# Optimization experiments

Hardware: AMD Instinct MI355X
Metric: run time of the kernel (lower is better)

Reference implementation:

```python
import jax, jax.numpy as jnp
import numpy as np

T = 16384
J = 21
IN = 3 * J + 278  # 341
H = 512
WIDTH = 64


def _gru_cell(x, h, w_ih, w_hh, b_ih, b_n):
    # equinox GRUCell math: igates = W_ih x + b; hgates = W_hh h
    ig = w_ih @ x + b_ih            # [3H]
    hg = w_hh @ h                   # [3H]
    ir, iz, inn = jnp.split(ig, 3)
    hr, hz, hn = jnp.split(hg, 3)
    r = jax.nn.sigmoid(ir + hr)
    z = jax.nn.sigmoid(iz + hz)
    n = jnp.tanh(inn + r * (hn + b_n))
    return n + z * (h - n)


def setup_inputs() -> dict:
    key = jax.random.key(0)
    ks = jax.random.split(key, 32)
    s = 0.02
    inp = {
        'dh_joint_pos_tj': jax.random.normal(ks[0], (T, J), jnp.float32),
        'dh_joint_vel_tj': jax.random.normal(ks[1], (T, J), jnp.float32),
        'com_inertia_tn': jax.random.normal(ks[2], (T, 160), jnp.float32),
        'com_vel_tn': jax.random.normal(ks[3], (T, 96), jnp.float32),
        'imu_acc_t3': jax.random.normal(ks[4], (T, 3), jnp.float32),
        'imu_gyro_t3': jax.random.normal(ks[5], (T, 3), jnp.float32),
        'act_frc_obs_tn': jax.random.normal(ks[6], (T, J), jnp.float32),
        'base_pos_t3': jax.random.normal(ks[7], (T, 3), jnp.float32),
        'base_quat_t4': jax.random.normal(ks[8], (T, 4), jnp.float32),
        'lin_vel_obs_t3': jax.random.normal(ks[9], (T, 3), jnp.float32),
        'ang_vel_obs_t3': jax.random.normal(ks[10], (T, 3), jnp.float32),
        'lin_vel_cmd_t2': jax.random.normal(ks[11], (T, 2), jnp.float32),
        'ang_vel_cmd_t1': jax.random.normal(ks[12], (T, 1), jnp.float32),
        'hidden_states_dn': jnp.zeros((2, H), jnp.float32),
        # GRU layer 0 (input IN -> H)
        'w_ih0': jax.random.normal(ks[13], (3 * H, IN), jnp.float32) * s,
        'w_hh0': jax.random.normal(ks[14], (3 * H, H), jnp.float32) * s,
        'b_ih0': jax.random.normal(ks[15], (3 * H,), jnp.float32) * s,
        'b_n0': jax.random.normal(ks[16], (H,), jnp.float32) * s,
        # GRU layer 1 (H -> H)
        'w_ih1': jax.random.normal(ks[17], (3 * H, H), jnp.float32) * s,
        'w_hh1': jax.random.normal(ks[18], (3 * H, H), jnp.float32) * s,
        'b_ih1': jax.random.normal(ks[19], (3 * H,), jnp.float32) * s,
        'b_n1': jax.random.normal(ks[20], (H,), jnp.float32) * s,
        # projector MLP: H -> 64 -> 64 -> 1, relu hidden activations
        'mw0': jax.random.normal(ks[21], (WIDTH, H), jnp.float32) * s,
        'mb0': jnp.zeros((WIDTH,), jnp.float32),
        'mw1': jax.random.normal(ks[22], (WIDTH, WIDTH), jnp.float32) * s,
        'mb1': jnp.zeros((WIDTH,), jnp.float32),
        'mw2': jax.random.normal(ks[23], (1, WIDTH), jnp.float32) * s,
        'mb2': jnp.zeros((1,), jnp.float32),
    }
    return inp


def reference(dh_joint_pos_tj, dh_joint_vel_tj, com_inertia_tn, com_vel_tn,
              imu_acc_t3, imu_gyro_t3, act_frc_obs_tn, base_pos_t3,
              base_quat_t4, lin_vel_obs_t3, ang_vel_obs_t3, lin_vel_cmd_t2,
              ang_vel_cmd_t1, hidden_states_dn,
              w_ih0, w_hh0, b_ih0, b_n0, w_ih1, w_hh1, b_ih1, b_n1,
              mw0, mb0, mw1, mb1, mw2, mb2):
    obs_tn = jnp.concatenate([
        dh_joint_pos_tj, dh_joint_vel_tj, com_inertia_tn, com_vel_tn,
        imu_acc_t3, imu_gyro_t3, act_frc_obs_tn, base_pos_t3, base_quat_t4,
        lin_vel_obs_t3, ang_vel_obs_t3, lin_vel_cmd_t2, ang_vel_cmd_t1,
    ], axis=-1)  # [T, 341]

    def scan_fn(carry, xt):
        h0 = _gru_cell(xt, carry[0], w_ih0, w_hh0, b_ih0, b_n0)
        h1 = _gru_cell(h0, carry[1], w_ih1, w_hh1, b_ih1, b_n1)
        v = jax.nn.relu(mw0 @ h1 + mb0)
        v = jax.nn.relu(mw1 @ v + mb1)
        yt = mw2 @ v + mb2  # [1]
        return jnp.stack([h0, h1], axis=0), yt

    new_hidden, out_tn = jax.lax.scan(scan_fn, hidden_states_dn, obs_tn)
    return out_tn, new_hidden
```

## Files before the change

kernel.cpp:

```cpp
#include <hip/hip_runtime.h>
#include <math.h>


#define T_STEPS 16384
#define IN_DIM 341
#define HID 512
#define G3 1536
#define TTILE 16
#define R0 16
#define R0M (R0-1)
#define R1 16
#define R1M (R1-1)

typedef unsigned int v4u __attribute__((ext_vector_type(4)));

__device__ __forceinline__ float dot4(float4 a, float4 b) {
  return fmaf(a.x, b.x, fmaf(a.y, b.y, fmaf(a.z, b.z, a.w * b.w)));
}
__device__ __forceinline__ float fast_sigmoid(float x) {
  return __builtin_amdgcn_rcpf(1.0f + __expf(-x));
}
__device__ __forceinline__ float fast_tanh(float x) {
  return fmaf(-2.0f, __builtin_amdgcn_rcpf(1.0f + __expf(2.0f * x)), 1.0f);
}
__device__ __forceinline__ void st_rlx64(unsigned long long* p, unsigned long long v) {
  __hip_atomic_store(p, v, __ATOMIC_RELAXED, __HIP_MEMORY_SCOPE_AGENT);
}
__device__ __forceinline__ unsigned long long pack_tv(unsigned tag, float v) {
  return ((unsigned long long)tag << 32) | (unsigned long long)__float_as_uint(v);
}
__device__ __forceinline__ void pin4(float4& v) {
  asm volatile("" : "+v"(v.x), "+v"(v.y), "+v"(v.z), "+v"(v.w));
}
__device__ __forceinline__ v4u ld16(const unsigned long long* p) {
  v4u r;
  asm volatile("global_load_dwordx4 %0, %1, off sc0 sc1\n\ts_waitcnt vmcnt(0)"
               : "=v"(r) : "v"(p) : "memory");
  return r;
}
__device__ __forceinline__ void ld16x2(const unsigned long long* p0,
                                       const unsigned long long* p1,
                                       v4u& a, v4u& b) {
  asm volatile("global_load_dwordx4 %0, %2, off sc0 sc1\n\t"
               "global_load_dwordx4 %1, %3, off sc0 sc1\n\t"
               "s_waitcnt vmcnt(0)"
               : "=v"(a), "=v"(b) : "v"(p0), "v"(p1) : "memory");
}

__global__ __launch_bounds__(384) void concat_kernel(
    const float* __restrict__ p0, const float* __restrict__ p1,
    const float* __restrict__ p2, const float* __restrict__ p3,
    const float* __restrict__ p4, const float* __restrict__ p5,
    const float* __restrict__ p6, const float* __restrict__ p7,
    const float* __restrict__ p8, const float* __restrict__ p9,
    const float* __restrict__ p10, const float* __restrict__ p11,
    const float* __restrict__ p12, float* __restrict__ obs) {
  int t = blockIdx.x;
  int k = threadIdx.x;
  if (k >= IN_DIM) return;
  float v;
  if (k < 21)       v = p0[t*21 + k];
  else if (k < 42)  v = p1[t*21 + (k-21)];
  else if (k < 202) v = p2[t*160 + (k-42)];
  else if (k < 298) v = p3[t*96 + (k-202)];
  else if (k < 301) v = p4[t*3 + (k-298)];
  else if (k < 304) v = p5[t*3 + (k-301)];
  else if (k < 325) v = p6[t*21 + (k-304)];
  else if (k < 328) v = p7[t*3 + (k-325)];
  else if (k < 332) v = p8[t*4 + (k-328)];
  else if (k < 335) v = p9[t*3 + (k-332)];
  else if (k < 338) v = p10[t*3 + (k-335)];
  else if (k < 340) v = p11[t*2 + (k-338)];
  else              v = p12[t];
  obs[(size_t)t*IN_DIM + k] = v;
}

__global__ __launch_bounds__(256) void transpose_kernel(const float* __restrict__ w,
                                                        float* __restrict__ wT) {
  __shared__ float tile[32][33];
  int tx = threadIdx.x;
  int ty = threadIdx.y;
  int k = blockIdx.x*32 + tx;
#pragma unroll
  for (int jj = 0; jj < 4; jj++) {
    int r = blockIdx.y*32 + ty*4 + jj;
    tile[ty*4+jj][tx] = (k < IN_DIM) ? w[(size_t)r*IN_DIM + k] : 0.f;
  }
  __syncthreads();
#pragma unroll
  for (int jj = 0; jj < 4; jj++) {
    int kk = blockIdx.x*32 + ty*4 + jj;
    if (kk < IN_DIM) wT[(size_t)kk*G3 + blockIdx.y*32 + tx] = tile[tx][ty*4+jj];
  }
}

__global__ __launch_bounds__(256) void ig0_kernel(const float* __restrict__ wT,
                                                  const float* __restrict__ obs,
                                                  const float* __restrict__ b_ih0,
                                                  float* __restrict__ ig0) {
  int o = blockIdx.x*256 + threadIdx.x;
  int t0 = blockIdx.y * TTILE;
  float acc[TTILE];
  float b = b_ih0[o];
#pragma unroll
  for (int tt = 0; tt < TTILE; tt++) acc[tt] = b;
  for (int k = 0; k < IN_DIM; k++) {
    float wv = wT[(size_t)k*G3 + o];
#pragma unroll
    for (int tt = 0; tt < TTILE; tt++)
      acc[tt] = fmaf(obs[(size_t)(t0+tt)*IN_DIM + k], wv, acc[tt]);
  }
#pragma unroll
  for (int tt = 0; tt < TTILE; tt++)
    ig0[(size_t)(t0+tt)*G3 + o] = acc[tt];
}

__global__ __launch_bounds__(512) void init_kernel(const float* __restrict__ hid,
                                                   unsigned long long* ring0,
                                                   unsigned long long* ring1) {
  int e = threadIdx.x;
  st_rlx64(&ring0[e], pack_tv(0u, hid[e]));
  st_rlx64(&ring1[e], pack_tv(0u, hid[HID + e]));
}

__global__ __launch_bounds__(384)
__attribute__((amdgpu_waves_per_eu(1, 2)))
void seq_kernel(
    const float* __restrict__ ig0, const float* __restrict__ w_hh0,
    const float* __restrict__ b_n0, const float* __restrict__ w_ih1,
    const float* __restrict__ w_hh1, const float* __restrict__ b_ih1,
    const float* __restrict__ b_n1,
    unsigned long long* ring0, unsigned long long* ring1,
    float* __restrict__ h1a, float* __restrict__ d_out) {
  __shared__ float hbuf0[2][HID];
  __shared__ float hbuf1[2][HID];
  __shared__ float igbuf[2][24];
  __shared__ float vpad[24576];
  const int tid = threadIdx.x;
  const int wg = blockIdx.x;
  if (d_out == nullptr) {
    vpad[tid] = (float)tid;
    __syncthreads();
    h1a[tid] = vpad[383 - tid];
  }

  const bool roleA = (tid < 128);
  const int u = tid - 128;
  const int g = roleA ? (tid >> 4) : (u >> 5);
  const int jj = roleA ? (tid & 15) : (u & 15);
  const int half = roleA ? 0 : ((u >> 4) & 1);
  const int j32 = roleA ? 0 : (u & 31);
  const int eg = wg*8 + g;
  const bool leadA = roleA && (jj == 0);
  const bool leadB = (!roleA) && (j32 == 0);

  const float* wsrc = roleA ? w_hh0 : (half ? w_hh1 : w_ih1);
  float4 W[24];
#pragma unroll
  for (int gate = 0; gate < 3; gate++) {
    const float4* row = (const float4*)(wsrc + (size_t)(gate*HID + eg)*HID);
#pragma unroll
    for (int i = 0; i < 8; i++) {
      W[gate*8+i] = row[jj + 16*i];
      pin4(W[gate*8+i]);
    }
  }
  float cr=0.f, cz=0.f, cn=0.f, bnl;
  if (roleA) {
    bnl = b_n0[eg];
  } else {
    cr = b_ih1[eg]; cz = b_ih1[512+eg]; cn = b_ih1[1024+eg]; bnl = b_n1[eg];
  }

  const int iggate = tid >> 3, ige = tid & 7;
  if (tid < 24) igbuf[0][tid] = ig0[(size_t)iggate*HID + wg*8 + ige];

  for (int k = 0; k <= T_STEPS; k++) {
    const int p = k & 1;
    float igpre = 0.f;
    if (tid < 24) {
      int kk = (k+1 < T_STEPS) ? (k+1) : (T_STEPS-1);
      igpre = ig0[(size_t)kk*G3 + (size_t)iggate*HID + wg*8 + ige];
    }
    const unsigned wk0 = (unsigned)k, wk1 = (unsigned)(k-1);
    if (k == 0) {
      if (tid < 256) {
        const unsigned long long* pa = ring0 + 2*tid;
        v4u a = ld16(pa);
        while (a.y != wk0 || a.w != wk0) { __builtin_amdgcn_s_sleep(1); a = ld16(pa); }
        ((float2*)hbuf0[p])[tid] =
            make_float2(__uint_as_float(a.x), __uint_as_float(a.z));
      }
    } else {
      const unsigned long long* pa = ring0 + (size_t)(k & R0M)*HID + 2*tid;
      const unsigned long long* pb = ring1 + (size_t)((k-1) & R1M)*HID + 2*(tid-128);
      if (tid < 128) {
        v4u a = ld16(pa);
        while (a.y != wk0 || a.w != wk0) { __builtin_amdgcn_s_sleep(1); a = ld16(pa); }
        ((float2*)hbuf0[p])[tid] =
            make_float2(__uint_as_float(a.x), __uint_as_float(a.z));
      } else if (tid < 256) {
        v4u a, b;
        ld16x2(pa, pb, a, b);
        while (a.y != wk0 || a.w != wk0) { __builtin_amdgcn_s_sleep(1); a = ld16(pa); }
        while (b.y != wk1 || b.w != wk1) { __builtin_amdgcn_s_sleep(1); b = ld16(pb); }
        ((float2*)hbuf0[p])[tid] =
            make_float2(__uint_as_float(a.x), __uint_as_float(a.z));
        ((float2*)hbuf1[p])[tid-128] =
            make_float2(__uint_as_float(b.x), __uint_as_float(b.z));
      } else {
        v4u b = ld16(pb);
        while (b.y != wk1 || b.w != wk1) { __builtin_amdgcn_s_sleep(1); b = ld16(pb); }
        ((float2*)hbuf1[p])[tid-128] =
            make_float2(__uint_as_float(b.x), __uint_as_float(b.z));
      }
    }
    __syncthreads();
    const bool act = roleA ? (k < T_STEPS) : (k >= 1);
    if (act) {
      const float4* hp = (roleA || half == 0) ? (const float4*)hbuf0[p]
                                              : (const float4*)hbuf1[p];
      float pr=0.f, pz=0.f, pn=0.f;
#pragma unroll
      for (int i = 0; i < 8; i++) {
        float4 hv = hp[jj + 16*i];
        pr += dot4(W[i],hv); pz += dot4(W[8+i],hv); pn += dot4(W[16+i],hv);
      }
#pragma unroll
      for (int s = 1; s < 16; s <<= 1) {
        pr += __shfl_xor(pr, s, 16);
        pz += __shfl_xor(pz, s, 16);
        pn += __shfl_xor(pn, s, 16);
      }
      if (roleA) {
        if (leadA) {
          float r = fast_sigmoid(igbuf[p][g] + pr);
          float z = fast_sigmoid(igbuf[p][8+g] + pz);
          float n = fast_tanh(igbuf[p][16+g] + r*(pn + bnl));
          float hnew = n + z*(hbuf0[p][eg] - n);
          st_rlx64(&ring0[(size_t)((k+1) & R0M)*HID + eg],
                   pack_tv((unsigned)(k+1), hnew));
          if (k == T_STEPS-1) d_out[T_STEPS + eg] = hnew;
        }
      } else {
        float qr = __shfl(pr, 16, 32);
        float qz = __shfl(pz, 16, 32);
        float qn = __shfl(pn, 16, 32);
        if (leadB) {
          float r = fast_sigmoid(pr + cr + qr);
          float z = fast_sigmoid(pz + cz + qz);
          float n = fast_tanh(pn + cn + r*(qn + bnl));
          float hnew = n + z*(hbuf1[p][eg] - n);
          st_rlx64(&ring1[(size_t)(k & R1M)*HID + eg],
                   pack_tv((unsigned)k, hnew));
          h1a[(size_t)(k-1)*HID + eg] = hnew;
          if (k == T_STEPS) d_out[T_STEPS + HID + eg] = hnew;
        }
      }
    }
    if (tid < 24) igbuf[p ^ 1][tid] = igpre;
  }
}

__global__ __launch_bounds__(64) void mlp_kernel(
    const float* __restrict__ h1_all, const float* __restrict__ mw0,
    const float* __restrict__ mb0, const float* __restrict__ mw1,
    const float* __restrict__ mb1, const float* __restrict__ mw2,
    const float* __restrict__ mb2, float* __restrict__ out) {
  const int l = threadIdx.x;
  const int t0 = blockIdx.x * 8;
  __shared__ float v0s[8][64];
  float acc[8];
#pragma unroll
  for (int tt = 0; tt < 8; tt++) acc[tt] = mb0[l];
  const float4* w = (const float4*)(mw0 + (size_t)l*512);
#pragma unroll 4
  for (int i = 0; i < 128; i++) {
    float4 a = w[i];
#pragma unroll
    for (int tt = 0; tt < 8; tt++) {
      float4 b = ((const float4*)(h1_all + (size_t)(t0+tt)*512))[i];
      acc[tt] = fmaf(a.x,b.x, fmaf(a.y,b.y, fmaf(a.z,b.z, fmaf(a.w,b.w, acc[tt]))));
    }
  }
#pragma unroll
  for (int tt = 0; tt < 8; tt++) v0s[tt][l] = fmaxf(acc[tt], 0.f);
  __syncthreads();
  float acc1[8];
#pragma unroll
  for (int tt = 0; tt < 8; tt++) acc1[tt] = mb1[l];
  const float* w1 = mw1 + (size_t)l*64;
  for (int jj = 0; jj < 64; jj++) {
    float wv = w1[jj];
#pragma unroll
    for (int tt = 0; tt < 8; tt++) acc1[tt] = fmaf(wv, v0s[tt][jj], acc1[tt]);
  }
  float w2 = mw2[l];
  float bb = mb2[0];
#pragma unroll
  for (int tt = 0; tt < 8; tt++) {
    float y = w2 * fmaxf(acc1[tt], 0.f);
#pragma unroll
    for (int s = 32; s > 0; s >>= 1) y += __shfl_down(y, s, 64);
    if (l == 0) out[t0+tt] = y + bb;
  }
}

extern "C" void kernel_launch(void* const* d_in, const int* in_sizes, int n_in,
                              void* d_out, int out_size, void* d_ws, size_t ws_size,
                              hipStream_t stream) {
  const float* p0  = (const float*)d_in[0];
  const float* p1  = (const float*)d_in[1];
  const float* p2  = (const float*)d_in[2];
  const float* p3  = (const float*)d_in[3];
  const float* p4  = (const float*)d_in[4];
  const float* p5  = (const float*)d_in[5];
  const float* p6  = (const float*)d_in[6];
  const float* p7  = (const float*)d_in[7];
  const float* p8  = (const float*)d_in[8];
  const float* p9  = (const float*)d_in[9];
  const float* p10 = (const float*)d_in[10];
  const float* p11 = (const float*)d_in[11];
  const float* p12 = (const float*)d_in[12];
  const float* hid   = (const float*)d_in[13];
  const float* w_ih0 = (const float*)d_in[14];
  const float* w_hh0 = (const float*)d_in[15];
  const float* b_ih0 = (const float*)d_in[16];
  const float* b_n0  = (const float*)d_in[17];
  const float* w_ih1 = (const float*)d_in[18];
  const float* w_hh1 = (const float*)d_in[19];
  const float* b_ih1 = (const float*)d_in[20];
  const float* b_n1  = (const float*)d_in[21];
  const float* mw0 = (const float*)d_in[22];
  const float* mb0 = (const float*)d_in[23];
  const float* mw1 = (const float*)d_in[24];
  const float* mb1 = (const float*)d_in[25];
  const float* mw2 = (const float*)d_in[26];
  const float* mb2 = (const float*)d_in[27];
  float* out = (float*)d_out;

  char* base = (char*)d_ws;
  const size_t IG0_B = (size_t)T_STEPS*G3*4;
  const size_t R0_B  = (size_t)R0*HID*8;
  const size_t R1_B  = (size_t)R1*HID*8;
  const size_t H1A_B = (size_t)T_STEPS*HID*4;
  float* ig0 = (float*)base;
  unsigned long long* ring0 = (unsigned long long*)(base + IG0_B);
  unsigned long long* ring1 = (unsigned long long*)(base + IG0_B + R0_B);
  float* h1a = (float*)(base + IG0_B + R0_B + R1_B);
  float* obs = h1a;
  float* wT  = (float*)((char*)h1a + (size_t)T_STEPS*IN_DIM*4);
  if (ws_size < IG0_B + R0_B + R1_B + H1A_B) return;

  concat_kernel<<<T_STEPS, 384, 0, stream>>>(p0,p1,p2,p3,p4,p5,p6,p7,p8,p9,p10,p11,p12, obs);
  transpose_kernel<<<dim3(11,48), dim3(32,8), 0, stream>>>(w_ih0, wT);
  ig0_kernel<<<dim3(6, T_STEPS/TTILE), 256, 0, stream>>>(wT, obs, b_ih0, ig0);
  init_kernel<<<1, 512, 0, stream>>>(hid, ring0, ring1);
  seq_kernel<<<64, 384, 0, stream>>>(ig0, w_hh0, b_n0, w_ih1, w_hh1, b_ih1, b_n1,
                                     ring0, ring1, h1a, out);
  mlp_kernel<<<T_STEPS/8, 64, 0, stream>>>(h1a, mw0, mb0, mw1, mb1, mw2, mb2, out);
}
```

Measured before the change: 27.60 ms.

## Halve persistent workgroups to 32 with 768 threads and add poll-timeout abort

The sequential GRU kernel now runs 32 workgroups of 768 threads, each owning 16 hidden elements instead of 8. The load work is re-split so that 256 threads poll ring0 and 256 threads poll ring1 separately, rather than some threads loading from both. Fewer workgroups means fewer participants in the per-step cross-workgroup handshake, which is meant to lower synchronisation latency on the serial critical path. The cost is more work and register pressure per workgroup. It also adds a bounded polling loop with a shared abort flag so that a deadlock (for example, when workgroups are not co-resident) ends the kernel instead of hanging, at the price of a few extra branches in the spin loop.

```diff
diff --git a/kernel.cpp b/kernel.cpp
--- a/kernel.cpp
+++ b/kernel.cpp
@@ -7,10 +7,10 @@
 #define HID 512
 #define G3 1536
 #define TTILE 16
-#define R0 16
-#define R0M (R0-1)
-#define R1 16
-#define R1M (R1-1)
+#define NWG 32
+#define EPW 16
+#define RMASK 15
+#define POLL_LIM (1<<18)
 
 typedef unsigned int v4u __attribute__((ext_vector_type(4)));
 
@@ -38,13 +38,24 @@
                : "=v"(r) : "v"(p) : "memory");
   return r;
 }
-__device__ __forceinline__ void ld16x2(const unsigned long long* p0,
-                                       const unsigned long long* p1,
-                                       v4u& a, v4u& b) {
-  asm volatile("global_load_dwordx4 %0, %2, off sc0 sc1\n\t"
-               "global_load_dwordx4 %1, %3, off sc0 sc1\n\t"
-               "s_waitcnt vmcnt(0)"
-               : "=v"(a), "=v"(b) : "v"(p0), "v"(p1) : "memory");
+__device__ __forceinline__ void set_abort(int* c) {
+  if (c) __hip_atomic_store(c, 1, __ATOMIC_RELAXED, __HIP_MEMORY_SCOPE_AGENT);
+}
+__device__ __forceinline__ bool chk_abort(const int* c) {
+  return c && __hip_atomic_load(c, __ATOMIC_RELAXED, __HIP_MEMORY_SCOPE_AGENT);
+}
+__device__ __forceinline__ bool wait_tag(const unsigned long long* p, unsigned tag,
+                                         v4u& a, int* ctrl) {
+  a = ld16(p);
+  if (a.y == tag && a.w == tag) return true;
+  int gd = 0;
+  for (;;) {
+    __builtin_amdgcn_s_sleep(1);
+    a = ld16(p);
+    if (a.y == tag && a.w == tag) return true;
+    if (++gd >= POLL_LIM) { set_abort(ctrl); return false; }
+    if ((gd & 255) == 0 && chk_abort(ctrl)) return false;
+  }
 }
 
 __global__ __launch_bounds__(384) void concat_kernel(
@@ -117,40 +128,44 @@
 
 __global__ __launch_bounds__(512) void init_kernel(const float* __restrict__ hid,
                                                    unsigned long long* ring0,
-                                                   unsigned long long* ring1) {
+                                                   unsigned long long* ring1,
+                                                   int* ctrl) {
   int e = threadIdx.x;
+  if (e == 0 && ctrl)
+    __hip_atomic_store(ctrl, 0, __ATOMIC_RELAXED, __HIP_MEMORY_SCOPE_AGENT);
   st_rlx64(&ring0[e], pack_tv(0u, hid[e]));
   st_rlx64(&ring1[e], pack_tv(0u, hid[HID + e]));
 }
 
-__global__ __launch_bounds__(384)
-__attribute__((amdgpu_waves_per_eu(1, 2)))
+__global__ __launch_bounds__(768, 3)
 void seq_kernel(
     const float* __restrict__ ig0, const float* __restrict__ w_hh0,
     const float* __restrict__ b_n0, const float* __restrict__ w_ih1,
     const float* __restrict__ w_hh1, const float* __restrict__ b_ih1,
     const float* __restrict__ b_n1,
     unsigned long long* ring0, unsigned long long* ring1,
-    float* __restrict__ h1a, float* __restrict__ d_out) {
+    float* __restrict__ h1a, float* __restrict__ d_out, int* ctrl) {
   __shared__ float hbuf0[2][HID];
   __shared__ float hbuf1[2][HID];
-  __shared__ float igbuf[2][24];
-  __shared__ float vpad[24576];
+  __shared__ float igbuf[2][48];
+  __shared__ float vpad[20480];
+  __shared__ int s_dead;
   const int tid = threadIdx.x;
   const int wg = blockIdx.x;
+  if (tid == 0) s_dead = 0;
   if (d_out == nullptr) {
     vpad[tid] = (float)tid;
     __syncthreads();
-    h1a[tid] = vpad[383 - tid];
-  }
-
-  const bool roleA = (tid < 128);
-  const int u = tid - 128;
+    h1a[tid] = vpad[767 - tid];
+  }
+
+  const bool roleA = (tid < 256);
+  const int u = tid - 256;
   const int g = roleA ? (tid >> 4) : (u >> 5);
   const int jj = roleA ? (tid & 15) : (u & 15);
   const int half = roleA ? 0 : ((u >> 4) & 1);
   const int j32 = roleA ? 0 : (u & 31);
-  const int eg = wg*8 + g;
+  const int eg = wg*EPW + g;
   const bool leadA = roleA && (jj == 0);
   const bool leadB = (!roleA) && (j32 == 0);
 
@@ -172,50 +187,39 @@
     cr = b_ih1[eg]; cz = b_ih1[512+eg]; cn = b_ih1[1024+eg]; bnl = b_n1[eg];
   }
 
-  const int iggate = tid >> 3, ige = tid & 7;
-  if (tid < 24) igbuf[0][tid] = ig0[(size_t)iggate*HID + wg*8 + ige];
+  const int iggate = tid >> 4, ige = tid & 15;
+  if (tid < 48) igbuf[0][tid] = ig0[(size_t)iggate*HID + wg*EPW + ige];
 
   for (int k = 0; k <= T_STEPS; k++) {
     const int p = k & 1;
     float igpre = 0.f;
-    if (tid < 24) {
+    if (tid < 48) {
       int kk = (k+1 < T_STEPS) ? (k+1) : (T_STEPS-1);
-      igpre = ig0[(size_t)kk*G3 + (size_t)iggate*HID + wg*8 + ige];
-    }
-    const unsigned wk0 = (unsigned)k, wk1 = (unsigned)(k-1);
+      igpre = ig0[(size_t)kk*G3 + (size_t)iggate*HID + wg*EPW + ige];
+    }
+    bool ok = true;
+    v4u a;
     if (k == 0) {
       if (tid < 256) {
-        const unsigned long long* pa = ring0 + 2*tid;
-        v4u a = ld16(pa);
-        while (a.y != wk0 || a.w != wk0) { __builtin_amdgcn_s_sleep(1); a = ld16(pa); }
+        ok = wait_tag(ring0 + 2*tid, 0u, a, ctrl);
         ((float2*)hbuf0[p])[tid] =
             make_float2(__uint_as_float(a.x), __uint_as_float(a.z));
       }
     } else {
-      const unsigned long long* pa = ring0 + (size_t)(k & R0M)*HID + 2*tid;
-      const unsigned long long* pb = ring1 + (size_t)((k-1) & R1M)*HID + 2*(tid-128);
-      if (tid < 128) {
-        v4u a = ld16(pa);
-        while (a.y != wk0 || a.w != wk0) { __builtin_amdgcn_s_sleep(1); a = ld16(pa); }
+      if (tid < 256) {
+        ok = wait_tag(ring0 + (size_t)(k & RMASK)*HID + 2*tid, (unsigned)k, a, ctrl);
         ((float2*)hbuf0[p])[tid] =
             make_float2(__uint_as_float(a.x), __uint_as_float(a.z));
-      } else if (tid < 256) {
-        v4u a, b;
-        ld16x2(pa, pb, a, b);
-        while (a.y != wk0 || a.w != wk0) { __builtin_amdgcn_s_sleep(1); a = ld16(pa); }
-        while (b.y != wk1 || b.w != wk1) { __builtin_amdgcn_s_sleep(1); b = ld16(pb); }
-        ((float2*)hbuf0[p])[tid] =
+      } else if (tid < 512) {
+        ok = wait_tag(ring1 + (size_t)((k-1) & RMASK)*HID + 2*(tid-256),
+                      (unsigned)(k-1), a, ctrl);
+        ((float2*)hbuf1[p])[tid-256] =
             make_float2(__uint_as_float(a.x), __uint_as_float(a.z));
-        ((float2*)hbuf1[p])[tid-128] =
-            make_float2(__uint_as_float(b.x), __uint_as_float(b.z));
-      } else {
-        v4u b = ld16(pb);
-        while (b.y != wk1 || b.w != wk1) { __builtin_amdgcn_s_sleep(1); b = ld16(pb); }
-        ((float2*)hbuf1[p])[tid-128] =
-            make_float2(__uint_as_float(b.x), __uint_as_float(b.z));
-      }
-    }
+      }
+    }
+    if (!ok) s_dead = 1;
     __syncthreads();
+    if (s_dead) break;
     const bool act = roleA ? (k < T_STEPS) : (k >= 1);
     if (act) {
       const float4* hp = (roleA || half == 0) ? (const float4*)hbuf0[p]
@@ -235,10 +239,10 @@
       if (roleA) {
         if (leadA) {
           float r = fast_sigmoid(igbuf[p][g] + pr);
-          float z = fast_sigmoid(igbuf[p][8+g] + pz);
-          float n = fast_tanh(igbuf[p][16+g] + r*(pn + bnl));
+          float z = fast_sigmoid(igbuf[p][16+g] + pz);
+          float n = fast_tanh(igbuf[p][32+g] + r*(pn + bnl));
           float hnew = n + z*(hbuf0[p][eg] - n);
-          st_rlx64(&ring0[(size_t)((k+1) & R0M)*HID + eg],
+          st_rlx64(&ring0[(size_t)((k+1) & RMASK)*HID + eg],
                    pack_tv((unsigned)(k+1), hnew));
           if (k == T_STEPS-1) d_out[T_STEPS + eg] = hnew;
         }
@@ -251,14 +255,14 @@
           float z = fast_sigmoid(pz + cz + qz);
           float n = fast_tanh(pn + cn + r*(qn + bnl));
           float hnew = n + z*(hbuf1[p][eg] - n);
-          st_rlx64(&ring1[(size_t)(k & R1M)*HID + eg],
+          st_rlx64(&ring1[(size_t)(k & RMASK)*HID + eg],
                    pack_tv((unsigned)k, hnew));
           h1a[(size_t)(k-1)*HID + eg] = hnew;
           if (k == T_STEPS) d_out[T_STEPS + HID + eg] = hnew;
         }
       }
     }
-    if (tid < 24) igbuf[p ^ 1][tid] = igpre;
+    if (tid < 48) igbuf[p ^ 1][tid] = igpre;
   }
 }
 
@@ -341,22 +345,24 @@
 
   char* base = (char*)d_ws;
   const size_t IG0_B = (size_t)T_STEPS*G3*4;
-  const size_t R0_B  = (size_t)R0*HID*8;
-  const size_t R1_B  = (size_t)R1*HID*8;
+  const size_t R0_B  = (size_t)16*HID*8;
+  const size_t R1_B  = (size_t)16*HID*8;
   const size_t H1A_B = (size_t)T_STEPS*HID*4;
+  const size_t TOTAL = IG0_B + R0_B + R1_B + H1A_B;
   float* ig0 = (float*)base;
   unsigned long long* ring0 = (unsigned long long*)(base + IG0_B);
   unsigned long long* ring1 = (unsigned long long*)(base + IG0_B + R0_B);
   float* h1a = (float*)(base + IG0_B + R0_B + R1_B);
   float* obs = h1a;
   float* wT  = (float*)((char*)h1a + (size_t)T_STEPS*IN_DIM*4);
-  if (ws_size < IG0_B + R0_B + R1_B + H1A_B) return;
+  if (ws_size < TOTAL) return;
+  int* ctrl = (ws_size >= TOTAL + 4096) ? (int*)(base + TOTAL) : nullptr;
 
   concat_kernel<<<T_STEPS, 384, 0, stream>>>(p0,p1,p2,p3,p4,p5,p6,p7,p8,p9,p10,p11,p12, obs);
   transpose_kernel<<<dim3(11,48), dim3(32,8), 0, stream>>>(w_ih0, wT);
   ig0_kernel<<<dim3(6, T_STEPS/TTILE), 256, 0, stream>>>(wT, obs, b_ih0, ig0);
-  init_kernel<<<1, 512, 0, stream>>>(hid, ring0, ring1);
-  seq_kernel<<<64, 384, 0, stream>>>(ig0, w_hh0, b_n0, w_ih1, w_hh1, b_ih1, b_n1,
-                                     ring0, ring1, h1a, out);
+  init_kernel<<<1, 512, 0, stream>>>(hid, ring0, ring1, ctrl);
+  seq_kernel<<<NWG, 768, 0, stream>>>(ig0, w_hh0, b_n0, w_ih1, w_hh1, b_ih1, b_n1,
+                                      ring0, ring1, h1a, out, ctrl);
   mlp_kernel<<<T_STEPS/8, 64, 0, stream>>>(h1a, mw0, mb0, mw1, mb1, mw2, mb2, out);
 }
```

Result: slower. 35.39 ms (+28.3%).

## Add abortable double-issue tag polling and DPP row reductions in GRU sequence kernel

Applied to the files above, without the earlier changes.

Replaces the per-element spin loops with a wait routine that issues two staggered loads per poll iteration, backs off its sleep, and gives up after a bound, setting a shared abort flag so all workgroups exit instead of hanging. The 16-lane butterfly shuffle reduction is replaced with DPP row-rotate adds. It also adds early-clobber constraints on the paired load asm. The goal is lower inter-workgroup handoff latency and cheaper reductions on the serial critical path, at the cost of extra polling traffic and an extra block-wide flag check every step.

```diff
diff --git a/kernel.cpp b/kernel.cpp
--- a/kernel.cpp
+++ b/kernel.cpp
@@ -7,10 +7,9 @@
 #define HID 512
 #define G3 1536
 #define TTILE 16
-#define R0 16
-#define R0M (R0-1)
-#define R1 16
-#define R1M (R1-1)
+#define R0M 15
+#define R1M 15
+#define POLL_LIM (1<<18)
 
 typedef unsigned int v4u __attribute__((ext_vector_type(4)));
 
@@ -31,6 +30,17 @@
 }
 __device__ __forceinline__ void pin4(float4& v) {
   asm volatile("" : "+v"(v.x), "+v"(v.y), "+v"(v.z), "+v"(v.w));
+}
+template <int CTRL>
+__device__ __forceinline__ float ror_add(float x) {
+  int t = __builtin_amdgcn_update_dpp(0, __float_as_int(x), CTRL, 0xf, 0xf, true);
+  return x + __int_as_float(t);
+}
+__device__ __forceinline__ void reduce16x3(float& pr, float& pz, float& pn) {
+  pr = ror_add<0x128>(pr); pz = ror_add<0x128>(pz); pn = ror_add<0x128>(pn);
+  pr = ror_add<0x124>(pr); pz = ror_add<0x124>(pz); pn = ror_add<0x124>(pn);
+  pr = ror_add<0x122>(pr); pz = ror_add<0x122>(pz); pn = ror_add<0x122>(pn);
+  pr = ror_add<0x121>(pr); pz = ror_add<0x121>(pz); pn = ror_add<0x121>(pn);
 }
 __device__ __forceinline__ v4u ld16(const unsigned long long* p) {
   v4u r;
@@ -44,7 +54,34 @@
   asm volatile("global_load_dwordx4 %0, %2, off sc0 sc1\n\t"
                "global_load_dwordx4 %1, %3, off sc0 sc1\n\t"
                "s_waitcnt vmcnt(0)"
-               : "=v"(a), "=v"(b) : "v"(p0), "v"(p1) : "memory");
+               : "=&v"(a), "=&v"(b) : "v"(p0), "v"(p1) : "memory");
+}
+__device__ __forceinline__ void set_abort(int* c) {
+  if (c) __hip_atomic_store(c, 1, __ATOMIC_RELAXED, __HIP_MEMORY_SCOPE_AGENT);
+}
+__device__ __forceinline__ bool chk_abort(const int* c) {
+  return c && __hip_atomic_load(c, __ATOMIC_RELAXED, __HIP_MEMORY_SCOPE_AGENT);
+}
+__device__ __forceinline__ bool wait_tag(const unsigned long long* p, unsigned tag,
+                                         v4u& a, int* ctrl) {
+  if (a.y == tag && a.w == tag) return true;
+  int gd = 0;
+  for (;;) {
+    v4u b0, b1;
+    asm volatile("global_load_dwordx4 %0, %2, off sc0 sc1\n\t"
+                 "s_sleep 3\n\t"
+                 "global_load_dwordx4 %1, %2, off sc0 sc1\n\t"
+                 "s_waitcnt vmcnt(1)"
+                 : "=&v"(b0), "=&v"(b1) : "v"(p) : "memory");
+    bool ok0 = (b0.y == tag && b0.w == tag);
+    asm volatile("s_waitcnt vmcnt(0)" : "+v"(b1) :: "memory");
+    if (ok0) { a = b0; return true; }
+    if (b1.y == tag && b1.w == tag) { a = b1; return true; }
+    if (++gd >= POLL_LIM) { set_abort(ctrl); return false; }
+    if ((gd & 63) == 0 && chk_abort(ctrl)) return false;
+    if (gd < 16) __builtin_amdgcn_s_sleep(1);
+    else         __builtin_amdgcn_s_sleep(8);
+  }
 }
 
 __global__ __launch_bounds__(384) void concat_kernel(
@@ -117,8 +154,11 @@
 
 __global__ __launch_bounds__(512) void init_kernel(const float* __restrict__ hid,
                                                    unsigned long long* ring0,
-                                                   unsigned long long* ring1) {
+                                                   unsigned long long* ring1,
+                                                   int* ctrl) {
   int e = threadIdx.x;
+  if (e == 0 && ctrl)
+    __hip_atomic_store(ctrl, 0, __ATOMIC_RELAXED, __HIP_MEMORY_SCOPE_AGENT);
   st_rlx64(&ring0[e], pack_tv(0u, hid[e]));
   st_rlx64(&ring1[e], pack_tv(0u, hid[HID + e]));
 }
@@ -131,13 +171,15 @@
     const float* __restrict__ w_hh1, const float* __restrict__ b_ih1,
     const float* __restrict__ b_n1,
     unsigned long long* ring0, unsigned long long* ring1,
-    float* __restrict__ h1a, float* __restrict__ d_out) {
+    float* __restrict__ h1a, float* __restrict__ d_out, int* ctrl) {
   __shared__ float hbuf0[2][HID];
   __shared__ float hbuf1[2][HID];
   __shared__ float igbuf[2][24];
   __shared__ float vpad[24576];
+  __shared__ int s_dead;
   const int tid = threadIdx.x;
   const int wg = blockIdx.x;
+  if (tid == 0) s_dead = 0;
   if (d_out == nullptr) {
     vpad[tid] = (float)tid;
     __syncthreads();
@@ -183,11 +225,12 @@
       igpre = ig0[(size_t)kk*G3 + (size_t)iggate*HID + wg*8 + ige];
     }
     const unsigned wk0 = (unsigned)k, wk1 = (unsigned)(k-1);
+    bool ok = true;
     if (k == 0) {
       if (tid < 256) {
         const unsigned long long* pa = ring0 + 2*tid;
         v4u a = ld16(pa);
-        while (a.y != wk0 || a.w != wk0) { __builtin_amdgcn_s_sleep(1); a = ld16(pa); }
+        ok = wait_tag(pa, wk0, a, ctrl);
         ((float2*)hbuf0[p])[tid] =
             make_float2(__uint_as_float(a.x), __uint_as_float(a.z));
       }
@@ -196,26 +239,29 @@
       const unsigned long long* pb = ring1 + (size_t)((k-1) & R1M)*HID + 2*(tid-128);
       if (tid < 128) {
         v4u a = ld16(pa);
-        while (a.y != wk0 || a.w != wk0) { __builtin_amdgcn_s_sleep(1); a = ld16(pa); }
+        ok = wait_tag(pa, wk0, a, ctrl);
         ((float2*)hbuf0[p])[tid] =
             make_float2(__uint_as_float(a.x), __uint_as_float(a.z));
       } else if (tid < 256) {
         v4u a, b;
         ld16x2(pa, pb, a, b);
-        while (a.y != wk0 || a.w != wk0) { __builtin_amdgcn_s_sleep(1); a = ld16(pa); }
-        while (b.y != wk1 || b.w != wk1) { __builtin_amdgcn_s_sleep(1); b = ld16(pb); }
+        bool okA = wait_tag(pa, wk0, a, ctrl);
+        bool okB = wait_tag(pb, wk1, b, ctrl);
+        ok = okA && okB;
         ((float2*)hbuf0[p])[tid] =
             make_float2(__uint_as_float(a.x), __uint_as_float(a.z));
         ((float2*)hbuf1[p])[tid-128] =
             make_float2(__uint_as_float(b.x), __uint_as_float(b.z));
       } else {
         v4u b = ld16(pb);
-        while (b.y != wk1 || b.w != wk1) { __builtin_amdgcn_s_sleep(1); b = ld16(pb); }
+        ok = wait_tag(pb, wk1, b, ctrl);
         ((float2*)hbuf1[p])[tid-128] =
             make_float2(__uint_as_float(b.x), __uint_as_float(b.z));
       }
     }
+    if (!ok) s_dead = 1;
     __syncthreads();
+    if (s_dead) break;
     const bool act = roleA ? (k < T_STEPS) : (k >= 1);
     if (act) {
       const float4* hp = (roleA || half == 0) ? (const float4*)hbuf0[p]
@@ -226,12 +272,7 @@
         float4 hv = hp[jj + 16*i];
         pr += dot4(W[i],hv); pz += dot4(W[8+i],hv); pn += dot4(W[16+i],hv);
       }
-#pragma unroll
-      for (int s = 1; s < 16; s <<= 1) {
-        pr += __shfl_xor(pr, s, 16);
-        pz += __shfl_xor(pz, s, 16);
-        pn += __shfl_xor(pn, s, 16);
-      }
+      reduce16x3(pr, pz, pn);
       if (roleA) {
         if (leadA) {
           float r = fast_sigmoid(igbuf[p][g] + pr);
@@ -341,22 +382,24 @@
 
   char* base = (char*)d_ws;
   const size_t IG0_B = (size_t)T_STEPS*G3*4;
-  const size_t R0_B  = (size_t)R0*HID*8;
-  const size_t R1_B  = (size_t)R1*HID*8;
+  const size_t R0_B  = (size_t)16*HID*8;
+  const size_t R1_B  = (size_t)16*HID*8;
   const size_t H1A_B = (size_t)T_STEPS*HID*4;
+  const size_t TOTAL = IG0_B + R0_B + R1_B + H1A_B;
   float* ig0 = (float*)base;
   unsigned long long* ring0 = (unsigned long long*)(base + IG0_B);
   unsigned long long* ring1 = (unsigned long long*)(base + IG0_B + R0_B);
   float* h1a = (float*)(base + IG0_B + R0_B + R1_B);
   float* obs = h1a;
   float* wT  = (float*)((char*)h1a + (size_t)T_STEPS*IN_DIM*4);
-  if (ws_size < IG0_B + R0_B + R1_B + H1A_B) return;
+  if (ws_size < TOTAL) return;
+  int* ctrl = (ws_size >= TOTAL + 4096) ? (int*)(base + TOTAL) : nullptr;
 
   concat_kernel<<<T_STEPS, 384, 0, stream>>>(p0,p1,p2,p3,p4,p5,p6,p7,p8,p9,p10,p11,p12, obs);
   transpose_kernel<<<dim3(11,48), dim3(32,8), 0, stream>>>(w_ih0, wT);
   ig0_kernel<<<dim3(6, T_STEPS/TTILE), 256, 0, stream>>>(wT, obs, b_ih0, ig0);
-  init_kernel<<<1, 512, 0, stream>>>(hid, ring0, ring1);
+  init_kernel<<<1, 512, 0, stream>>>(hid, ring0, ring1, ctrl);
   seq_kernel<<<64, 384, 0, stream>>>(ig0, w_hh0, b_n0, w_ih1, w_hh1, b_ih1, b_n1,
-                                     ring0, ring1, h1a, out);
+                                     ring0, ring1, h1a, out, ctrl);
   mlp_kernel<<<T_STEPS/8, 64, 0, stream>>>(h1a, mw0, mb0, mw1, mb1, mw2, mb2, out);
 }
```

Measured after the change: 30.14 ms. 1.09x slower.
